# Kernel tuning notes

Measured on AMD Instinct MI355X. Metric: run time of the kernel, lower is better.

The kernel has to match this reference:

```python
import jax, jax.numpy as jnp
import numpy as np
import math

B, M, N = 1, 128, 256
LIG_C = 256      # rep_1d num_c
ATTN_C = 32      # attention_num_c
HEADS = 8        # num_heads
EPS = 1e-5


def setup_inputs() -> dict:
    key = jax.random.key(0)
    ks = jax.random.split(key, 8)
    s = 1.0 / math.sqrt(LIG_C)
    return {
        "lig_profile": jax.random.normal(ks[0], (B, M, N, LIG_C), dtype=jnp.float32),
        "ln_scale": jnp.ones((LIG_C,), dtype=jnp.float32),
        "ln_bias": jnp.zeros((LIG_C,), dtype=jnp.float32),
        "wq": jax.random.normal(ks[1], (LIG_C, ATTN_C * HEADS), dtype=jnp.float32) * s,
        "wk": jax.random.normal(ks[2], (LIG_C, ATTN_C * HEADS), dtype=jnp.float32) * s,
        "wv": jax.random.normal(ks[3], (LIG_C, ATTN_C * HEADS), dtype=jnp.float32) * s,
        "wf": jax.random.normal(ks[4], (ATTN_C * HEADS, LIG_C), dtype=jnp.float32) * s,
        "bf": jnp.zeros((LIG_C,), dtype=jnp.float32),
    }


def reference(lig_profile, ln_scale, ln_bias, wq, wk, wv, wf, bf):
    # LayerNorm over channel dim
    mu = jnp.mean(lig_profile, axis=-1, keepdims=True)
    var = jnp.mean(jnp.square(lig_profile - mu), axis=-1, keepdims=True)
    x = (lig_profile - mu) * jax.lax.rsqrt(var + EPS) * ln_scale + ln_bias

    # QKV projections; view splits last dim as (attn_c, heads) -> channel-major layout
    shape5 = x.shape[:-1] + (ATTN_C, HEADS)
    q = (x @ wq).reshape(shape5)  # [b,m,n,c,h]
    k = (x @ wk).reshape(shape5)
    v = (x @ wv).reshape(shape5)

    factor = 1.0 / math.sqrt(ATTN_C)
    aff = jnp.einsum('bmich,bmjch->bmijh', q, k) * factor  # [b,m,i,j,h]
    weights = jax.nn.softmax(aff, axis=-2)                  # softmax over j (keys)
    out = jnp.einsum('bmrch,bmirh->bmich', v, weights)      # [b,m,i,c,h]
    out = out.reshape(out.shape[:-2] + (ATTN_C * HEADS,))
    return out @ wf + bf
```

## Files before the change

kernel.cpp:

```cpp
#include <hip/hip_runtime.h>

typedef _Float16 f16;
typedef _Float16 f16x8 __attribute__((ext_vector_type(8)));
typedef _Float16 f16x4 __attribute__((ext_vector_type(4)));
typedef _Float16 f16x2 __attribute__((ext_vector_type(2)));
typedef float f32x4 __attribute__((ext_vector_type(4)));
typedef float f32x16 __attribute__((ext_vector_type(16)));

#define MDIM 128
#define NDIM 256
#define CDIM 256
#define ROWS (MDIM*NDIM)
#define L2E 1.4426950408889634f

__device__ inline int pk2(float a, float b) {
  union { f16x2 h; int i; } u;
  u.h[0] = (f16)a; u.h[1] = (f16)b;
  return u.i;
}

__global__ __launch_bounds__(256) void k_prep(
    const float* __restrict__ wq, const float* __restrict__ wk,
    const float* __restrict__ wv, const float* __restrict__ wf,
    f16* __restrict__ bq, f16* __restrict__ bk, f16* __restrict__ bv,
    f16* __restrict__ bw)
{
  __shared__ f16 ld[64][264];
  int which = blockIdx.x >> 2, kb = blockIdx.x & 3;
  int t = threadIdx.x;
  int k0 = kb * 64;
  if (which < 3) {
    const float* W = which == 0 ? wq : which == 1 ? wk : wv;
    f16* dst       = which == 0 ? bq : which == 1 ? bk : bv;
    float sc = which == 0 ? 0.17677669529663689f : 1.0f;
    for (int r = 0; r < 64; ++r)
      ld[r][t] = (f16)(W[(size_t)(k0 + r) * 256 + t] * sc);
    __syncthreads();
    int j = (t & 31) * 8 + (t >> 5);
#pragma unroll
    for (int rr = 0; rr < 8; ++rr) {
      f16x8 o;
#pragma unroll
      for (int i = 0; i < 8; ++i) o[i] = ld[rr * 8 + i][j];
      *(f16x8*)(dst + (size_t)t * 256 + k0 + rr * 8) = o;
    }
  } else {
    for (int r = 0; r < 64; ++r) {
      int ke = k0 + r;
      int jr = (ke & 31) * 8 + (ke >> 5);
      ld[r][t] = (f16)wf[(size_t)jr * 256 + t];
    }
    __syncthreads();
#pragma unroll
    for (int rr = 0; rr < 8; ++rr) {
      f16x8 o;
#pragma unroll
      for (int i = 0; i < 8; ++i) o[i] = ld[rr * 8 + i][t];
      *(f16x8*)(bw + (size_t)t * 256 + k0 + rr * 8) = o;
    }
  }
}

__global__ __launch_bounds__(256) void k_ln(const float* __restrict__ x,
                                            const float* __restrict__ g,
                                            const float* __restrict__ b,
                                            f16* __restrict__ y)
{
  int row  = blockIdx.x * 4 + (threadIdx.x >> 6);
  int lane = threadIdx.x & 63;
  const float4 xv = *(const float4*)(x + (size_t)row * CDIM + lane * 4);
  float s  = xv.x + xv.y + xv.z + xv.w;
  float s2 = xv.x*xv.x + xv.y*xv.y + xv.z*xv.z + xv.w*xv.w;
#pragma unroll
  for (int m = 1; m < 64; m <<= 1) {
    s  += __shfl_xor(s,  m, 64);
    s2 += __shfl_xor(s2, m, 64);
  }
  float mu  = s * (1.0f / CDIM);
  float var = s2 * (1.0f / CDIM) - mu * mu;
  float rs  = rsqrtf(var + 1e-5f);
  const float4 gv = *(const float4*)(g + lane * 4);
  const float4 bv = *(const float4*)(b + lane * 4);
  f16x4 o;
  o[0] = (f16)((xv.x - mu) * rs * gv.x + bv.x);
  o[1] = (f16)((xv.y - mu) * rs * gv.y + bv.y);
  o[2] = (f16)((xv.z - mu) * rs * gv.z + bv.z);
  o[3] = (f16)((xv.w - mu) * rs * gv.w + bv.w);
  *(f16x4*)(y + (size_t)row * CDIM + lane * 4) = o;
}

__global__ __launch_bounds__(256, 4) void k_qkv(const f16* __restrict__ xh,
    const f16* __restrict__ bq, const f16* __restrict__ bk, const f16* __restrict__ bv,
    f16* __restrict__ qo, f16* __restrict__ ko, f16* __restrict__ vT)
{
  __shared__ f16 Bs[64][264];
  __shared__ f16 vtmp[64][72];
  int bm = blockIdx.x;
  int sec = blockIdx.y;
  const f16* B = sec == 0 ? bq : sec == 1 ? bk : bv;
  int t = threadIdx.x, lane = t & 63, w = t >> 6;
  int l15 = lane & 15, l4 = lane >> 4;
  int r0 = bm * 64 + w * 16;
  int pr = t >> 2, pc = (t & 3) * 8;
  f16x8 af[8];
#pragma unroll
  for (int kt = 0; kt < 8; ++kt)
    af[kt] = *(const f16x8*)(xh + (size_t)(r0 + l15) * 256 + kt * 32 + l4 * 8);
  for (int ct = 0; ct < 4; ++ct) {
#pragma unroll
    for (int p = 0; p < 8; ++p)
      *(f16x8*)&Bs[pr][pc + p * 32] =
        *(const f16x8*)(B + (size_t)(ct * 64 + pr) * 256 + pc + p * 32);
    __syncthreads();
    f32x4 acc[4] = {};
#pragma unroll
    for (int kt = 0; kt < 8; ++kt) {
#pragma unroll
      for (int ni = 0; ni < 4; ++ni) {
        f16x8 bf = *(const f16x8*)&Bs[ni * 16 + l15][kt * 32 + l4 * 8];
        acc[ni] = __builtin_amdgcn_mfma_f32_16x16x32_f16(af[kt], bf, acc[ni], 0, 0, 0);
      }
    }
    if (sec < 2) {
      f16* dst = sec == 0 ? qo : ko;
#pragma unroll
      for (int ni = 0; ni < 4; ++ni)
#pragma unroll
        for (int r = 0; r < 4; ++r)
          dst[(size_t)(r0 + l4 * 4 + r) * 256 + ct * 64 + ni * 16 + l15] = (f16)acc[ni][r];
      __syncthreads();
    } else {
#pragma unroll
      for (int ni = 0; ni < 4; ++ni)
#pragma unroll
        for (int r = 0; r < 4; ++r)
          vtmp[ni * 16 + l15][w * 16 + l4 * 4 + r] = (f16)acc[ni][r];
      __syncthreads();
      int ch = t >> 2, nq = (t & 3) * 16;
      int m = bm >> 2, n0 = (bm & 3) * 64;
      size_t gd = ((size_t)m * 256 + ct * 64 + ch) * 256 + n0 + nq;
      *(f16x8*)(vT + gd)     = *(const f16x8*)&vtmp[ch][nq];
      *(f16x8*)(vT + gd + 8) = *(const f16x8*)&vtmp[ch][nq + 8];
      __syncthreads();
    }
  }
}

__global__ __launch_bounds__(512, 4) void k_attn(const f16* __restrict__ q,
    const f16* __restrict__ k, const f16* __restrict__ vT, f16* __restrict__ o)
{
  __shared__ f16 ks[256][40];
  __shared__ f16 vt[32][264];
  int bx = blockIdx.x;
  int m = bx >> 3, h = bx & 7;
  int t = threadIdx.x, lane = t & 63, w = t >> 6;
  int i32 = lane & 31, hi = lane >> 5;
  size_t rowbase = (size_t)m * 256;
#pragma unroll
  for (int p = 0; p < 2; ++p) {
    int n = p * 128 + (t >> 2);
    int c0 = (t & 3) * 8;
    *(f16x8*)&ks[n][c0] = *(const f16x8*)(k + (rowbase + n) * 256 + h * 32 + c0);
  }
#pragma unroll
  for (int p = 0; p < 2; ++p) {
    int idx = p * 512 + t;
    int c = idx >> 5, nb = (idx & 31) * 8;
    *(f16x8*)&vt[c][nb] = *(const f16x8*)(vT + ((size_t)m * 256 + h * 32 + c) * 256 + nb);
  }
  __syncthreads();
  int qi0 = w * 32;
  const f16* qp = q + (rowbase + qi0 + i32) * 256 + h * 32 + hi * 8;
  f16x8 qf0 = *(const f16x8*)(qp);
  f16x8 qf1 = *(const f16x8*)(qp + 16);
  f32x16 O = {};
  float m_run = -1e30f, l_run = 0.f;
#pragma unroll 2
  for (int kb = 0; kb < 8; ++kb) {
    f16x8 kf0 = *(const f16x8*)&ks[kb * 32 + i32][hi * 8];
    f16x8 kf1 = *(const f16x8*)&ks[kb * 32 + i32][16 + hi * 8];
    f32x16 s = {};
    __builtin_amdgcn_s_setprio(1);
    s = __builtin_amdgcn_mfma_f32_32x32x16_f16(kf0, qf0, s, 0, 0, 0);
    s = __builtin_amdgcn_mfma_f32_32x32x16_f16(kf1, qf1, s, 0, 0, 0);
    __builtin_amdgcn_s_setprio(0);
#pragma unroll
    for (int r = 0; r < 16; ++r) s[r] *= L2E;
    float pmax = s[0];
#pragma unroll
    for (int r = 1; r < 16; ++r) pmax = fmaxf(pmax, s[r]);
    pmax = fmaxf(pmax, __shfl_xor(pmax, 32, 64));
    if (!__all(pmax - m_run <= 8.f)) {
      float m_new = fmaxf(m_run, pmax);
      float f = __builtin_amdgcn_exp2f(m_run - m_new);
      l_run *= f;
#pragma unroll
      for (int r = 0; r < 16; ++r)
        O[r] *= __shfl(f, (r & 3) + 8 * (r >> 2) + 4 * hi, 64);
      m_run = m_new;
    }
    float lsum = 0.f;
#pragma unroll
    for (int r = 0; r < 16; ++r) {
      float e = __builtin_amdgcn_exp2f(s[r] - m_run);
      s[r] = e;
      lsum += e;
    }
    lsum += __shfl_xor(lsum, 32, 64);
    l_run += lsum;
    int W0[4], W1[4];
#pragma unroll
    for (int qq = 0; qq < 4; ++qq) {
      W0[qq] = pk2(s[4 * qq],     s[4 * qq + 1]);
      W1[qq] = pk2(s[4 * qq + 2], s[4 * qq + 3]);
    }
#pragma unroll
    for (int ks2 = 0; ks2 < 2; ++ks2) {
      int X0 = W0[2 * ks2], Y0 = W0[2 * ks2 + 1];
      int X1 = W1[2 * ks2], Y1 = W1[2 * ks2 + 1];
      int a0 = __shfl(X0, i32, 64),      b0 = __shfl(Y0, i32, 64);
      int a1 = __shfl(X1, i32, 64),      b1 = __shfl(Y1, i32, 64);
      int a2 = __shfl(X0, i32 + 32, 64), b2 = __shfl(Y0, i32 + 32, 64);
      int a3 = __shfl(X1, i32 + 32, 64), b3 = __shfl(Y1, i32 + 32, 64);
      union { unsigned int ww[4]; f16x8 v; } pa;
      pa.ww[0] = hi ? (unsigned)b0 : (unsigned)a0;
      pa.ww[1] = hi ? (unsigned)b1 : (unsigned)a1;
      pa.ww[2] = hi ? (unsigned)b2 : (unsigned)a2;
      pa.ww[3] = hi ? (unsigned)b3 : (unsigned)a3;
      f16x8 vb = *(const f16x8*)&vt[i32][kb * 32 + ks2 * 16 + hi * 8];
      __builtin_amdgcn_s_setprio(1);
      O = __builtin_amdgcn_mfma_f32_32x32x16_f16(pa.v, vb, O, 0, 0, 0);
      __builtin_amdgcn_s_setprio(0);
    }
  }
  float inv = 1.f / l_run;
#pragma unroll
  for (int r = 0; r < 16; ++r) {
    int i = (r & 3) + 8 * (r >> 2) + 4 * hi;
    float fr = __shfl(inv, i, 64);
    o[(rowbase + (size_t)(qi0 + i)) * 256 + h * 32 + i32] = (f16)(O[r] * fr);
  }
}

__global__ __launch_bounds__(256, 4) void k_out(const f16* __restrict__ a,
    const f16* __restrict__ bw, const float* __restrict__ bias,
    float* __restrict__ out)
{
  __shared__ f16 Bs[64][264];
  int bm = blockIdx.x;
  int half = blockIdx.y;
  int t = threadIdx.x, lane = t & 63, w = t >> 6;
  int l15 = lane & 15, l4 = lane >> 4;
  int r0 = bm * 64 + w * 16;
  int pr = t >> 2, pc = (t & 3) * 8;
  f16x8 af[8];
#pragma unroll
  for (int kt = 0; kt < 8; ++kt)
    af[kt] = *(const f16x8*)(a + (size_t)(r0 + l15) * 256 + kt * 32 + l4 * 8);
  for (int ct = 0; ct < 2; ++ct) {
    int col0 = half * 128 + ct * 64;
#pragma unroll
    for (int p = 0; p < 8; ++p)
      *(f16x8*)&Bs[pr][pc + p * 32] =
        *(const f16x8*)(bw + (size_t)(col0 + pr) * 256 + pc + p * 32);
    __syncthreads();
    f32x4 acc[4] = {};
#pragma unroll
    for (int kt = 0; kt < 8; ++kt) {
#pragma unroll
      for (int ni = 0; ni < 4; ++ni) {
        f16x8 bf = *(const f16x8*)&Bs[ni * 16 + l15][kt * 32 + l4 * 8];
        acc[ni] = __builtin_amdgcn_mfma_f32_16x16x32_f16(af[kt], bf, acc[ni], 0, 0, 0);
      }
    }
#pragma unroll
    for (int ni = 0; ni < 4; ++ni) {
      float bv = bias[col0 + ni * 16 + l15];
#pragma unroll
      for (int r = 0; r < 4; ++r)
        out[(size_t)(r0 + l4 * 4 + r) * 256 + col0 + ni * 16 + l15] = acc[ni][r] + bv;
    }
    __syncthreads();
  }
}

extern "C" void kernel_launch(void* const* d_in, const int* in_sizes, int n_in,
                              void* d_out, int out_size, void* d_ws, size_t ws_size,
                              hipStream_t stream)
{
  const float* x  = (const float*)d_in[0];
  const float* g  = (const float*)d_in[1];
  const float* b  = (const float*)d_in[2];
  const float* wq = (const float*)d_in[3];
  const float* wk = (const float*)d_in[4];
  const float* wv = (const float*)d_in[5];
  const float* wf = (const float*)d_in[6];
  const float* bf = (const float*)d_in[7];
  float* out = (float*)d_out;

  char* ws = (char*)d_ws;
  f16* xh  = (f16*)(ws);
  f16* qh  = (f16*)(ws + (size_t)16 * 1024 * 1024);
  f16* kh  = (f16*)(ws + (size_t)32 * 1024 * 1024);
  f16* vTh = (f16*)(ws + (size_t)48 * 1024 * 1024);
  char* wbase = ws + (size_t)64 * 1024 * 1024;
  f16* bq = (f16*)(wbase);
  f16* bk = (f16*)(wbase + 128 * 1024);
  f16* bv = (f16*)(wbase + 256 * 1024);
  f16* bw = (f16*)(wbase + 384 * 1024);
  f16* ah = (f16*)(ws + (size_t)80 * 1024 * 1024);

  k_prep<<<16,           256, 0, stream>>>(wq, wk, wv, wf, bq, bk, bv, bw);
  k_ln  <<<ROWS / 4,     256, 0, stream>>>(x, g, b, xh);
  k_qkv <<<dim3(512, 3), 256, 0, stream>>>(xh, bq, bk, bv, qh, kh, vTh);
  k_attn<<<1024,         512, 0, stream>>>(qh, kh, vTh, ah);
  k_out <<<dim3(512, 2), 256, 0, stream>>>(ah, bw, bf, out);
}
```

Baseline: 88.73 us.

## Restructure QKV and output GEMMs to keep weight tile resident across row tiles

```diff
diff --git a/kernel.cpp b/kernel.cpp
--- a/kernel.cpp
+++ b/kernel.cpp
@@ -25,39 +25,41 @@
     f16* __restrict__ bq, f16* __restrict__ bk, f16* __restrict__ bv,
     f16* __restrict__ bw)
 {
-  __shared__ f16 ld[64][264];
-  int which = blockIdx.x >> 2, kb = blockIdx.x & 3;
+  __shared__ f16 ld[16][264];
+  int which = blockIdx.x >> 4, kb = blockIdx.x & 15;
   int t = threadIdx.x;
-  int k0 = kb * 64;
+  int k0 = kb * 16;
   if (which < 3) {
     const float* W = which == 0 ? wq : which == 1 ? wk : wv;
     f16* dst       = which == 0 ? bq : which == 1 ? bk : bv;
     float sc = which == 0 ? 0.17677669529663689f : 1.0f;
-    for (int r = 0; r < 64; ++r)
+#pragma unroll
+    for (int r = 0; r < 16; ++r)
       ld[r][t] = (f16)(W[(size_t)(k0 + r) * 256 + t] * sc);
     __syncthreads();
     int j = (t & 31) * 8 + (t >> 5);
-#pragma unroll
-    for (int rr = 0; rr < 8; ++rr) {
-      f16x8 o;
-#pragma unroll
-      for (int i = 0; i < 8; ++i) o[i] = ld[rr * 8 + i][j];
-      *(f16x8*)(dst + (size_t)t * 256 + k0 + rr * 8) = o;
-    }
+    f16x8 o;
+#pragma unroll
+    for (int i = 0; i < 8; ++i) o[i] = ld[i][j];
+    *(f16x8*)(dst + (size_t)t * 256 + k0) = o;
+#pragma unroll
+    for (int i = 0; i < 8; ++i) o[i] = ld[8 + i][j];
+    *(f16x8*)(dst + (size_t)t * 256 + k0 + 8) = o;
   } else {
-    for (int r = 0; r < 64; ++r) {
+#pragma unroll
+    for (int r = 0; r < 16; ++r) {
       int ke = k0 + r;
       int jr = (ke & 31) * 8 + (ke >> 5);
       ld[r][t] = (f16)wf[(size_t)jr * 256 + t];
     }
     __syncthreads();
-#pragma unroll
-    for (int rr = 0; rr < 8; ++rr) {
-      f16x8 o;
-#pragma unroll
-      for (int i = 0; i < 8; ++i) o[i] = ld[rr * 8 + i][t];
-      *(f16x8*)(bw + (size_t)t * 256 + k0 + rr * 8) = o;
-    }
+    f16x8 o;
+#pragma unroll
+    for (int i = 0; i < 8; ++i) o[i] = ld[i][t];
+    *(f16x8*)(bw + (size_t)t * 256 + k0) = o;
+#pragma unroll
+    for (int i = 0; i < 8; ++i) o[i] = ld[8 + i][t];
+    *(f16x8*)(bw + (size_t)t * 256 + k0 + 8) = o;
   }
 }
 
@@ -89,29 +91,34 @@
   *(f16x4*)(y + (size_t)row * CDIM + lane * 4) = o;
 }
 
-__global__ __launch_bounds__(256, 4) void k_qkv(const f16* __restrict__ xh,
+__global__ __launch_bounds__(256) void k_qkv(const f16* __restrict__ xh,
     const f16* __restrict__ bq, const f16* __restrict__ bk, const f16* __restrict__ bv,
     f16* __restrict__ qo, f16* __restrict__ ko, f16* __restrict__ vT)
 {
   __shared__ f16 Bs[64][264];
-  __shared__ f16 vtmp[64][72];
-  int bm = blockIdx.x;
-  int sec = blockIdx.y;
+  __shared__ f16 vtmp[4][64][18];
+  int mp = blockIdx.x;
+  int nc = blockIdx.y;
+  int sec = nc >> 2;
+  int c0  = (nc & 3) * 64;
   const f16* B = sec == 0 ? bq : sec == 1 ? bk : bv;
+  f16* dst     = sec == 0 ? qo : ko;
   int t = threadIdx.x, lane = t & 63, w = t >> 6;
   int l15 = lane & 15, l4 = lane >> 4;
-  int r0 = bm * 64 + w * 16;
-  int pr = t >> 2, pc = (t & 3) * 8;
-  f16x8 af[8];
-#pragma unroll
-  for (int kt = 0; kt < 8; ++kt)
-    af[kt] = *(const f16x8*)(xh + (size_t)(r0 + l15) * 256 + kt * 32 + l4 * 8);
-  for (int ct = 0; ct < 4; ++ct) {
+  {
+    int pr = t >> 2, pc = (t & 3) * 8;
 #pragma unroll
     for (int p = 0; p < 8; ++p)
       *(f16x8*)&Bs[pr][pc + p * 32] =
-        *(const f16x8*)(B + (size_t)(ct * 64 + pr) * 256 + pc + p * 32);
-    __syncthreads();
+        *(const f16x8*)(B + (size_t)(c0 + pr) * 256 + pc + p * 32);
+  }
+  __syncthreads();
+  for (int it = 0; it < 4; ++it) {
+    int r0 = mp * 256 + it * 64 + w * 16;
+    f16x8 af[8];
+#pragma unroll
+    for (int kt = 0; kt < 8; ++kt)
+      af[kt] = *(const f16x8*)(xh + (size_t)(r0 + l15) * 256 + kt * 32 + l4 * 8);
     f32x4 acc[4] = {};
 #pragma unroll
     for (int kt = 0; kt < 8; ++kt) {
@@ -122,26 +129,23 @@
       }
     }
     if (sec < 2) {
-      f16* dst = sec == 0 ? qo : ko;
 #pragma unroll
       for (int ni = 0; ni < 4; ++ni)
 #pragma unroll
         for (int r = 0; r < 4; ++r)
-          dst[(size_t)(r0 + l4 * 4 + r) * 256 + ct * 64 + ni * 16 + l15] = (f16)acc[ni][r];
-      __syncthreads();
+          dst[(size_t)(r0 + l4 * 4 + r) * 256 + c0 + ni * 16 + l15] = (f16)acc[ni][r];
     } else {
 #pragma unroll
       for (int ni = 0; ni < 4; ++ni)
 #pragma unroll
         for (int r = 0; r < 4; ++r)
-          vtmp[ni * 16 + l15][w * 16 + l4 * 4 + r] = (f16)acc[ni][r];
-      __syncthreads();
-      int ch = t >> 2, nq = (t & 3) * 16;
-      int m = bm >> 2, n0 = (bm & 3) * 64;
-      size_t gd = ((size_t)m * 256 + ct * 64 + ch) * 256 + n0 + nq;
-      *(f16x8*)(vT + gd)     = *(const f16x8*)&vtmp[ch][nq];
-      *(f16x8*)(vT + gd + 8) = *(const f16x8*)&vtmp[ch][nq + 8];
-      __syncthreads();
+          vtmp[w][ni * 16 + l15][l4 * 4 + r] = (f16)acc[ni][r];
+      int n0 = it * 64 + w * 16;
+      f16x8 v0 = *(const f16x8*)&vtmp[w][lane][0];
+      f16x8 v1 = *(const f16x8*)&vtmp[w][lane][8];
+      size_t gd = ((size_t)mp * 256 + c0 + lane) * 256 + n0;
+      *(f16x8*)(vT + gd)     = v0;
+      *(f16x8*)(vT + gd + 8) = v1;
     }
   }
 }
@@ -242,28 +246,33 @@
   }
 }
 
-__global__ __launch_bounds__(256, 4) void k_out(const f16* __restrict__ a,
+__global__ __launch_bounds__(256) void k_out(const f16* __restrict__ a,
     const f16* __restrict__ bw, const float* __restrict__ bias,
     float* __restrict__ out)
 {
   __shared__ f16 Bs[64][264];
-  int bm = blockIdx.x;
-  int half = blockIdx.y;
+  int mp = blockIdx.x;
+  int nc = blockIdx.y;
+  int c0 = nc * 64;
   int t = threadIdx.x, lane = t & 63, w = t >> 6;
   int l15 = lane & 15, l4 = lane >> 4;
-  int r0 = bm * 64 + w * 16;
-  int pr = t >> 2, pc = (t & 3) * 8;
-  f16x8 af[8];
-#pragma unroll
-  for (int kt = 0; kt < 8; ++kt)
-    af[kt] = *(const f16x8*)(a + (size_t)(r0 + l15) * 256 + kt * 32 + l4 * 8);
-  for (int ct = 0; ct < 2; ++ct) {
-    int col0 = half * 128 + ct * 64;
+  {
+    int pr = t >> 2, pc = (t & 3) * 8;
 #pragma unroll
     for (int p = 0; p < 8; ++p)
       *(f16x8*)&Bs[pr][pc + p * 32] =
-        *(const f16x8*)(bw + (size_t)(col0 + pr) * 256 + pc + p * 32);
-    __syncthreads();
+        *(const f16x8*)(bw + (size_t)(c0 + pr) * 256 + pc + p * 32);
+  }
+  __syncthreads();
+  float bv[4];
+#pragma unroll
+  for (int ni = 0; ni < 4; ++ni) bv[ni] = bias[c0 + ni * 16 + l15];
+  for (int it = 0; it < 4; ++it) {
+    int r0 = mp * 256 + it * 64 + w * 16;
+    f16x8 af[8];
+#pragma unroll
+    for (int kt = 0; kt < 8; ++kt)
+      af[kt] = *(const f16x8*)(a + (size_t)(r0 + l15) * 256 + kt * 32 + l4 * 8);
     f32x4 acc[4] = {};
 #pragma unroll
     for (int kt = 0; kt < 8; ++kt) {
@@ -274,13 +283,10 @@
       }
     }
 #pragma unroll
-    for (int ni = 0; ni < 4; ++ni) {
-      float bv = bias[col0 + ni * 16 + l15];
+    for (int ni = 0; ni < 4; ++ni)
 #pragma unroll
       for (int r = 0; r < 4; ++r)
-        out[(size_t)(r0 + l4 * 4 + r) * 256 + col0 + ni * 16 + l15] = acc[ni][r] + bv;
-    }
-    __syncthreads();
+        out[(size_t)(r0 + l4 * 4 + r) * 256 + c0 + ni * 16 + l15] = acc[ni][r] + bv[ni];
   }
 }
 
@@ -310,9 +316,9 @@
   f16* bw = (f16*)(wbase + 384 * 1024);
   f16* ah = (f16*)(ws + (size_t)80 * 1024 * 1024);
 
-  k_prep<<<16,           256, 0, stream>>>(wq, wk, wv, wf, bq, bk, bv, bw);
-  k_ln  <<<ROWS / 4,     256, 0, stream>>>(x, g, b, xh);
-  k_qkv <<<dim3(512, 3), 256, 0, stream>>>(xh, bq, bk, bv, qh, kh, vTh);
-  k_attn<<<1024,         512, 0, stream>>>(qh, kh, vTh, ah);
-  k_out <<<dim3(512, 2), 256, 0, stream>>>(ah, bw, bf, out);
-}
+  k_prep<<<64,            256, 0, stream>>>(wq, wk, wv, wf, bq, bk, bv, bw);
+  k_ln  <<<ROWS / 4,      256, 0, stream>>>(x, g, b, xh);
+  k_qkv <<<dim3(128, 12), 256, 0, stream>>>(xh, bq, bk, bv, qh, kh, vTh);
+  k_attn<<<1024,          512, 0, stream>>>(qh, kh, vTh, ah);
+  k_out <<<dim3(128, 4),  256, 0, stream>>>(ah, bw, bf, out);
+}
```

Result: slower. 95.07 us (+7.1%).
